# Kernel tuning notes

Hardware: AMD Instinct MI355X
Metric: run time of the kernel (lower is better)

## Reference

```python
import jax, jax.numpy as jnp
import numpy as np

D = 128
N = 768
EPS = 1e-5

def _layernorm(x, w, b):
    m = jnp.mean(x, axis=-1, keepdims=True)
    v = jnp.mean(jnp.square(x - m), axis=-1, keepdims=True)
    return (x - m) * jax.lax.rsqrt(v + EPS) * w + b

def _linear(x, w, b):
    # torch Linear convention: w is [out, in]
    return jnp.einsum('...i,oi->...o', x, w) + b

def setup_inputs() -> dict:
    key = jax.random.key(0)
    ks = jax.random.split(key, 8)
    s = 1.0 / np.sqrt(D)
    d = {
        'pair': jax.random.normal(ks[0], (N, N, D), dtype=jnp.float32),
        'ln_in_w': jnp.ones((D,), jnp.float32), 'ln_in_b': jnp.zeros((D,), jnp.float32),
        'lp_w': jax.random.uniform(ks[1], (D, D), jnp.float32, -s, s), 'lp_b': jnp.zeros((D,), jnp.float32),
        'lg_w': jax.random.uniform(ks[2], (D, D), jnp.float32, -s, s), 'lg_b': jnp.zeros((D,), jnp.float32),
        'rp_w': jax.random.uniform(ks[3], (D, D), jnp.float32, -s, s), 'rp_b': jnp.zeros((D,), jnp.float32),
        'rg_w': jax.random.uniform(ks[4], (D, D), jnp.float32, -s, s), 'rg_b': jnp.zeros((D,), jnp.float32),
        'cn_w': jnp.ones((D,), jnp.float32), 'cn_b': jnp.zeros((D,), jnp.float32),
        'op_w': jax.random.uniform(ks[5], (D, D), jnp.float32, -s, s), 'op_b': jnp.zeros((D,), jnp.float32),
        'og_w': jax.random.uniform(ks[6], (D, D), jnp.float32, -s, s), 'og_b': jnp.zeros((D,), jnp.float32),
        'ln_out_w': jnp.ones((D,), jnp.float32), 'ln_out_b': jnp.zeros((D,), jnp.float32),
    }
    return d

def reference(pair, ln_in_w, ln_in_b, lp_w, lp_b, lg_w, lg_b, rp_w, rp_b, rg_w, rg_b,
              cn_w, cn_b, op_w, op_b, og_w, og_b, ln_out_w, ln_out_b):
    z = _layernorm(pair, ln_in_w, ln_in_b)
    left = jax.nn.sigmoid(_linear(z, lg_w, lg_b)) * _linear(z, lp_w, lp_b)
    right = jax.nn.sigmoid(_linear(z, rg_w, rg_b)) * _linear(z, rp_w, rp_b)
    # outgoing direction: pair(i,j) = sum_k left(i,k,d) * right(j,k,d)
    tri = jnp.einsum('ikd,jkd->ijd', left, right)
    tri = _layernorm(tri, cn_w, cn_b)
    tri = jax.nn.sigmoid(_linear(pair, og_w, og_b)) * _linear(tri, op_w, op_b)
    return _layernorm(pair + tri, ln_out_w, ln_out_b)
```

## Files before the change

kernel.cpp:

```cpp
#include <hip/hip_runtime.h>

#define N 768
#define D 128
#define NSQ (N*N)
#define EPS 1e-5f

typedef __bf16 bf16;
typedef __bf16 bf16x4 __attribute__((ext_vector_type(4)));
typedef __bf16 bf16x8 __attribute__((ext_vector_type(8)));
typedef float f32x4 __attribute__((ext_vector_type(4)));

__device__ __forceinline__ void gld16(const void* g, void* l) {
    __builtin_amdgcn_global_load_lds(
        (const __attribute__((address_space(1))) unsigned int*)g,
        (__attribute__((address_space(3))) unsigned int*)l, 16, 0, 0);
}

__global__ void k_convert_w(const float* __restrict__ lp, const float* __restrict__ lg,
                            const float* __restrict__ rp, const float* __restrict__ rg,
                            const float* __restrict__ op, const float* __restrict__ og,
                            bf16* __restrict__ dst) {
    const float* srcs[6] = {lp, lg, rp, rg, op, og};
    int m = blockIdx.y;
    int i = blockIdx.x * 256 + threadIdx.x;
    dst[m * 16384 + i] = (bf16)srcs[m][i];
}

__global__ __launch_bounds__(512, 2) void k_ln_gate2(
    const float* __restrict__ pair, const float* __restrict__ lnw, const float* __restrict__ lnb,
    const bf16* __restrict__ wbf,
    const float* __restrict__ lp_b, const float* __restrict__ lg_b,
    const float* __restrict__ rp_b, const float* __restrict__ rg_b,
    bf16* __restrict__ left_t, bf16* __restrict__ right_t)
{
    __shared__ bf16 zt[2][64 * 128];

    const int t = threadIdx.x;
    const int lane = t & 63, wid = t >> 6;
    const int side = wid >> 2, dq = wid & 3;
    const int lr = lane & 15, lh = lane >> 4;

    const bf16* wPsrc = wbf + (side ? 2 : 0) * 16384;
    const bf16* wGsrc = wbf + (side ? 3 : 1) * 16384;
    const float* bPp = side ? rp_b : lp_b;
    const float* bGp = side ? rg_b : lg_b;
    bf16* dst = side ? right_t : left_t;

    bf16x8 aP[4][2], aG[4][2];
    #pragma unroll
    for (int kk = 0; kk < 4; ++kk)
        #pragma unroll
        for (int m = 0; m < 2; ++m) {
            int rd = dq * 32 + m * 16 + lr;
            aP[kk][m] = *(const bf16x8*)(wPsrc + rd * 128 + (kk * 4 + lh) * 8);
            aG[kk][m] = *(const bf16x8*)(wGsrc + rd * 128 + (kk * 4 + lh) * 8);
        }
    float bP[2], bG[2];
    #pragma unroll
    for (int m = 0; m < 2; ++m) {
        bP[m] = bPp[dq * 32 + m * 16 + lr];
        bG[m] = bGp[dq * 32 + m * 16 + lr];
    }

    const int r8 = t >> 3, q = t & 7;

    f32x4 lw0 = *(const f32x4*)(lnw + q * 16);
    f32x4 lw1 = *(const f32x4*)(lnw + q * 16 + 4);
    f32x4 lw2 = *(const f32x4*)(lnw + q * 16 + 8);
    f32x4 lw3 = *(const f32x4*)(lnw + q * 16 + 12);
    f32x4 lb0 = *(const f32x4*)(lnb + q * 16);
    f32x4 lb1 = *(const f32x4*)(lnb + q * 16 + 4);
    f32x4 lb2 = *(const f32x4*)(lnb + q * 16 + 8);
    f32x4 lb3 = *(const f32x4*)(lnb + q * 16 + 12);

    const int bid = blockIdx.x, gstride = gridDim.x;

    f32x4 p0, p1, p2, p3;
    {
        const float* prow = pair + (size_t)(bid * 64 + r8) * 128 + q * 16;
        p0 = *(const f32x4*)(prow);
        p1 = *(const f32x4*)(prow + 4);
        p2 = *(const f32x4*)(prow + 8);
        p3 = *(const f32x4*)(prow + 12);
    }

    int buf = 0;
    for (int tile = bid; tile < NSQ / 64; tile += gstride) {
        const int row0 = tile * 64;

        float x[16];
        #pragma unroll
        for (int e = 0; e < 4; ++e) {
            x[e] = p0[e]; x[4 + e] = p1[e]; x[8 + e] = p2[e]; x[12 + e] = p3[e];
        }
        float s1 = 0.f, s2 = 0.f;
        #pragma unroll
        for (int j = 0; j < 16; ++j) { s1 += x[j]; s2 += x[j] * x[j]; }
        s1 += __shfl_xor(s1, 1); s2 += __shfl_xor(s2, 1);
        s1 += __shfl_xor(s1, 2); s2 += __shfl_xor(s2, 2);
        s1 += __shfl_xor(s1, 4); s2 += __shfl_xor(s2, 4);
        float mean = s1 * (1.f / 128.f);
        float rstd = rsqrtf(s2 * (1.f / 128.f) - mean * mean + EPS);

        bf16x8 pk0, pk1;
        #pragma unroll
        for (int e = 0; e < 4; ++e) {
            pk0[e]     = (bf16)((x[e]      - mean) * rstd * lw0[e] + lb0[e]);
            pk0[4 + e] = (bf16)((x[4 + e]  - mean) * rstd * lw1[e] + lb1[e]);
            pk1[e]     = (bf16)((x[8 + e]  - mean) * rstd * lw2[e] + lb2[e]);
            pk1[4 + e] = (bf16)((x[12 + e] - mean) * rstd * lw3[e] + lb3[e]);
        }
        {
            char* zb = (char*)&zt[buf][0];
            *(bf16x8*)(zb + r8 * 256 + ((q * 2)     ^ (r8 & 7)) * 16) = pk0;
            *(bf16x8*)(zb + r8 * 256 + ((q * 2 + 1) ^ (r8 & 7)) * 16) = pk1;
        }
        __syncthreads();

        int nt = tile + gstride;
        if (nt < NSQ / 64) {
            const float* prow = pair + (size_t)(nt * 64 + r8) * 128 + q * 16;
            p0 = *(const f32x4*)(prow);
            p1 = *(const f32x4*)(prow + 4);
            p2 = *(const f32x4*)(prow + 8);
            p3 = *(const f32x4*)(prow + 12);
        }

        f32x4 accP[2][4] = {};
        f32x4 accG[2][4] = {};
        const char* zb = (const char*)&zt[buf][0];
        #pragma unroll
        for (int kk = 0; kk < 4; ++kk) {
            bf16x8 bz[4];
            #pragma unroll
            for (int n = 0; n < 4; ++n) {
                int rz = n * 16 + lr;
                bz[n] = *(const bf16x8*)(zb + rz * 256 + (((kk * 4 + lh)) ^ (rz & 7)) * 16);
            }
            #pragma unroll
            for (int m = 0; m < 2; ++m)
                #pragma unroll
                for (int n = 0; n < 4; ++n) {
                    accP[m][n] = __builtin_amdgcn_mfma_f32_16x16x32_bf16(bz[n], aP[kk][m], accP[m][n], 0, 0, 0);
                    accG[m][n] = __builtin_amdgcn_mfma_f32_16x16x32_bf16(bz[n], aG[kk][m], accG[m][n], 0, 0, 0);
                }
        }

        #pragma unroll
        for (int m = 0; m < 2; ++m) {
            const int d = dq * 32 + m * 16 + lr;
            bf16* drow = dst + (size_t)d * NSQ + row0 + lh * 4;
            #pragma unroll
            for (int n = 0; n < 4; ++n) {
                bf16x4 pk;
                #pragma unroll
                for (int reg = 0; reg < 4; ++reg) {
                    float g = accG[m][n][reg] + bG[m];
                    float p = accP[m][n][reg] + bP[m];
                    pk[reg] = (bf16)(p * (1.f / (1.f + __expf(-g))));
                }
                *(bf16x4*)(drow + n * 16) = pk;
            }
        }
        buf ^= 1;
        __syncthreads();
    }
}

__global__ __launch_bounds__(256, 4) void k_tri(
    const bf16* __restrict__ left_t, const bf16* __restrict__ right_t, bf16* __restrict__ tri_t)
{
    __shared__ bf16 at[2][128 * 32];
    __shared__ bf16 bt[2][128 * 32];
    const int t = threadIdx.x;
    const int b = blockIdx.x;
    const int xcd = b & 7;
    const int s = b >> 3;
    const int d = xcd * 16 + s / 36;
    const int tile = s % 36;
    const int ti = tile / 6, tj = tile % 6;
    const bf16* A = left_t + (size_t)d * NSQ;
    const bf16* B = right_t + (size_t)d * NSQ;
    const int i0 = ti * 128, j0 = tj * 128;

    auto stage = [&](int buf, int kt) {
        int k0 = kt * 32;
        #pragma unroll
        for (int c = 0; c < 2; ++c) {
            int sl = c * 256 + t;
            int r = sl >> 2, cp = sl & 3, cl = cp ^ ((r >> 1) & 3);
            gld16(A + (size_t)(i0 + r) * 768 + k0 + cl * 8, (char*)at[buf] + sl * 16);
            gld16(B + (size_t)(j0 + r) * 768 + k0 + cl * 8, (char*)bt[buf] + sl * 16);
        }
    };

    const int lane = t & 63, wid = t >> 6;
    const int wr = wid >> 1, wc = wid & 1;
    const int lr = lane & 15, lh = lane >> 4;

    f32x4 acc[4][4] = {};

    stage(0, 0);
    for (int kt = 0; kt < 24; ++kt) {
        const int buf = kt & 1;
        asm volatile("s_waitcnt vmcnt(0)" ::: "memory");
        __builtin_amdgcn_s_barrier();

        const bf16* ab = at[buf];
        const bf16* bb = bt[buf];
        bf16x8 af[4], bff[4];
        #pragma unroll
        for (int m = 0; m < 4; ++m) {
            int r = wr * 64 + m * 16 + lr;
            int phys = lh ^ ((r >> 1) & 3);
            af[m] = *(const bf16x8*)((const char*)ab + r * 64 + phys * 16);
        }
        #pragma unroll
        for (int n = 0; n < 4; ++n) {
            int r = wc * 64 + n * 16 + lr;
            int phys = lh ^ ((r >> 1) & 3);
            bff[n] = *(const bf16x8*)((const char*)bb + r * 64 + phys * 16);
        }

        if (kt < 23) stage(buf ^ 1, kt + 1);

        #pragma unroll
        for (int m = 0; m < 4; ++m)
            #pragma unroll
            for (int n = 0; n < 4; ++n)
                acc[m][n] = __builtin_amdgcn_mfma_f32_16x16x32_bf16(bff[n], af[m], acc[m][n], 0, 0, 0);
    }

    bf16* C = tri_t + (size_t)d * NSQ;
    #pragma unroll
    for (int m = 0; m < 4; ++m) {
        const int ri = i0 + wr * 64 + m * 16 + lr;
        bf16* crow = C + (size_t)ri * 768 + j0 + wc * 64 + lh * 4;
        #pragma unroll
        for (int n = 0; n < 4; ++n) {
            bf16x4 pk;
            #pragma unroll
            for (int reg = 0; reg < 4; ++reg)
                pk[reg] = (bf16)acc[m][n][reg];
            *(bf16x4*)(crow + n * 16) = pk;
        }
    }
}

__global__ __launch_bounds__(256, 2) void k_cln(
    const bf16* __restrict__ tri_t, const float* __restrict__ cnw, const float* __restrict__ cnb,
    bf16* __restrict__ tri_ln)
{
    __shared__ bf16 tile[256 * 128];
    __shared__ float mrs[256][2];
    const int t = threadIdx.x;
    const size_t ij = (size_t)blockIdx.x * 256 + t;
    float s1 = 0.f, s2 = 0.f;
    for (int dc = 0; dc < 16; ++dc) {
        bf16x8 pk;
        #pragma unroll
        for (int e = 0; e < 8; ++e) {
            int dd = dc * 8 + e;
            bf16 raw = tri_t[(size_t)dd * NSQ + ij];
            float v = (float)raw;
            s1 += v; s2 += v * v;
            pk[e] = raw;
        }
        *(bf16x8*)((char*)tile + t * 256 + (dc ^ (t & 7)) * 16) = pk;
    }
    float mean = s1 * (1.f / 128.f);
    float rstd = rsqrtf(s2 * (1.f / 128.f) - mean * mean + EPS);
    mrs[t][0] = mean; mrs[t][1] = rstd;
    __syncthreads();
    const size_t ij0 = (size_t)blockIdx.x * 256;
    #pragma unroll
    for (int c = 0; c < 16; ++c) {
        int sl = c * 256 + t;
        int rl = sl >> 4, cp = sl & 15, cl = cp ^ (rl & 7);
        bf16x8 raw = *(const bf16x8*)((const char*)tile + rl * 256 + cp * 16);
        float m = mrs[rl][0], r = mrs[rl][1];
        f32x4 w0 = *(const f32x4*)(cnw + cl * 8);
        f32x4 w1 = *(const f32x4*)(cnw + cl * 8 + 4);
        f32x4 b0 = *(const f32x4*)(cnb + cl * 8);
        f32x4 b1 = *(const f32x4*)(cnb + cl * 8 + 4);
        bf16x8 o;
        #pragma unroll
        for (int e = 0; e < 4; ++e) {
            o[e]     = (bf16)(((float)raw[e]     - m) * r * w0[e] + b0[e]);
            o[4 + e] = (bf16)(((float)raw[4 + e] - m) * r * w1[e] + b1[e]);
        }
        *(bf16x8*)(tri_ln + (ij0 + rl) * 128 + cl * 8) = o;
    }
}

__global__ __launch_bounds__(512, 2) void k_final2(
    const float* __restrict__ pair, const bf16* __restrict__ tri_ln,
    const bf16* __restrict__ wbf,
    const float* __restrict__ op_b, const float* __restrict__ og_b,
    const float* __restrict__ lnow, const float* __restrict__ lnob,
    float* __restrict__ out)
{
    __shared__ bf16 zt[64 * 128];
    __shared__ bf16 tt[2][64 * 128];
    __shared__ bf16 ub[64 * 136];

    const int t = threadIdx.x;
    const int lane = t & 63, wid = t >> 6;
    const int dq = wid & 3, wh = wid >> 2;
    const int lr = lane & 15, lh = lane >> 4;

    const bf16* opsrc = wbf + 4 * 16384;
    const bf16* ogsrc = wbf + 5 * 16384;

    bf16x8 aOG[4][2], aOP[4][2];
    #pragma unroll
    for (int kk = 0; kk < 4; ++kk)
        #pragma unroll
        for (int m = 0; m < 2; ++m) {
            int rd = dq * 32 + m * 16 + lr;
            aOG[kk][m] = *(const bf16x8*)(ogsrc + rd * 128 + (kk * 4 + lh) * 8);
            aOP[kk][m] = *(const bf16x8*)(opsrc + rd * 128 + (kk * 4 + lh) * 8);
        }
    f32x4 vbOG[2], vbOP[2];
    #pragma unroll
    for (int m = 0; m < 2; ++m) {
        vbOG[m] = *(const f32x4*)(og_b + dq * 32 + m * 16 + lh * 4);
        vbOP[m] = *(const f32x4*)(op_b + dq * 32 + m * 16 + lh * 4);
    }

    const int r8 = t >> 3, q = t & 7;
    f32x4 lw0 = *(const f32x4*)(lnow + q * 16);
    f32x4 lw1 = *(const f32x4*)(lnow + q * 16 + 4);
    f32x4 lw2 = *(const f32x4*)(lnow + q * 16 + 8);
    f32x4 lw3 = *(const f32x4*)(lnow + q * 16 + 12);
    f32x4 lb0 = *(const f32x4*)(lnob + q * 16);
    f32x4 lb1 = *(const f32x4*)(lnob + q * 16 + 4);
    f32x4 lb2 = *(const f32x4*)(lnob + q * 16 + 8);
    f32x4 lb3 = *(const f32x4*)(lnob + q * 16 + 12);

    const int bid = blockIdx.x, gstride = gridDim.x;

    auto stage_tt = [&](int buf, int tile) {
        const int row0 = tile * 64;
        #pragma unroll
        for (int c = 0; c < 2; ++c) {
            int s = c * 512 + t;
            int r = s >> 4, cp = s & 15, cl = cp ^ (r & 7);
            gld16(tri_ln + (size_t)(row0 + r) * 128 + cl * 8, (char*)tt[buf] + s * 16);
        }
    };

    f32x4 pA0, pA1, pA2, pA3;
    {
        const float* prow = pair + (size_t)(bid * 64 + r8) * 128 + q * 16;
        pA0 = *(const f32x4*)(prow);
        pA1 = *(const f32x4*)(prow + 4);
        pA2 = *(const f32x4*)(prow + 8);
        pA3 = *(const f32x4*)(prow + 12);
    }
    stage_tt(0, bid);

    int buf = 0;
    for (int tile = bid; tile < NSQ / 64; tile += gstride) {
        const int row0 = tile * 64;

        {
            bf16x8 pk0, pk1;
            #pragma unroll
            for (int e = 0; e < 4; ++e) {
                pk0[e]     = (bf16)pA0[e];
                pk0[4 + e] = (bf16)pA1[e];
                pk1[e]     = (bf16)pA2[e];
                pk1[4 + e] = (bf16)pA3[e];
            }
            char* zb = (char*)zt;
            *(bf16x8*)(zb + r8 * 256 + ((q * 2)     ^ (r8 & 7)) * 16) = pk0;
            *(bf16x8*)(zb + r8 * 256 + ((q * 2 + 1) ^ (r8 & 7)) * 16) = pk1;
        }
        __syncthreads();

        const int nt = tile + gstride;
        if (nt < NSQ / 64) stage_tt(buf ^ 1, nt);

        f32x4 pB0 = pA0, pB1 = pA1, pB2 = pA2, pB3 = pA3;
        if (nt < NSQ / 64) {
            const float* prow = pair + (size_t)(nt * 64 + r8) * 128 + q * 16;
            pB0 = *(const f32x4*)(prow);
            pB1 = *(const f32x4*)(prow + 4);
            pB2 = *(const f32x4*)(prow + 8);
            pB3 = *(const f32x4*)(prow + 12);
        }

        f32x4 accOG[2][2] = {};
        f32x4 accOP[2][2] = {};
        const char* zb = (const char*)zt;
        const char* tb = (const char*)tt[buf];
        #pragma unroll
        for (int kk = 0; kk < 4; ++kk) {
            bf16x8 bzp[2], bzt[2];
            #pragma unroll
            for (int n = 0; n < 2; ++n) {
                int rz = wh * 32 + n * 16 + lr;
                int phys = (kk * 4 + lh) ^ (rz & 7);
                bzp[n] = *(const bf16x8*)(zb + rz * 256 + phys * 16);
                bzt[n] = *(const bf16x8*)(tb + rz * 256 + phys * 16);
            }
            #pragma unroll
            for (int m = 0; m < 2; ++m)
                #pragma unroll
                for (int n = 0; n < 2; ++n) {
                    accOG[m][n] = __builtin_amdgcn_mfma_f32_16x16x32_bf16(aOG[kk][m], bzp[n], accOG[m][n], 0, 0, 0);
                    accOP[m][n] = __builtin_amdgcn_mfma_f32_16x16x32_bf16(aOP[kk][m], bzt[n], accOP[m][n], 0, 0, 0);
                }
        }

        #pragma unroll
        for (int m = 0; m < 2; ++m)
            #pragma unroll
            for (int n = 0; n < 2; ++n) {
                int rr = wh * 32 + n * 16 + lr;
                bf16x4 v;
                #pragma unroll
                for (int reg = 0; reg < 4; ++reg) {
                    float g = accOG[m][n][reg] + vbOG[m][reg];
                    float p = accOP[m][n][reg] + vbOP[m][reg];
                    v[reg] = (bf16)(p * (1.f / (1.f + __expf(-g))));
                }
                *(bf16x4*)(ub + rr * 136 + dq * 32 + m * 16 + lh * 4) = v;
            }
        __syncthreads();

        {
            float x[16];
            const bf16* ur = ub + r8 * 136 + q * 16;
            bf16x8 u0 = *(const bf16x8*)(ur);
            bf16x8 u1 = *(const bf16x8*)(ur + 8);
            #pragma unroll
            for (int e = 0; e < 4; ++e) {
                x[e]      = pA0[e] + (float)u0[e];
                x[4 + e]  = pA1[e] + (float)u0[4 + e];
                x[8 + e]  = pA2[e] + (float)u1[e];
                x[12 + e] = pA3[e] + (float)u1[4 + e];
            }
            float s1 = 0.f, s2 = 0.f;
            #pragma unroll
            for (int j = 0; j < 16; ++j) { s1 += x[j]; s2 += x[j] * x[j]; }
            s1 += __shfl_xor(s1, 1); s2 += __shfl_xor(s2, 1);
            s1 += __shfl_xor(s1, 2); s2 += __shfl_xor(s2, 2);
            s1 += __shfl_xor(s1, 4); s2 += __shfl_xor(s2, 4);
            float mean = s1 * (1.f / 128.f);
            float rstd = rsqrtf(s2 * (1.f / 128.f) - mean * mean + EPS);
            float* orow = out + (size_t)(row0 + r8) * 128 + q * 16;
            f32x4 o0, o1, o2, o3;
            #pragma unroll
            for (int e = 0; e < 4; ++e) {
                o0[e] = (x[e]      - mean) * rstd * lw0[e] + lb0[e];
                o1[e] = (x[4 + e]  - mean) * rstd * lw1[e] + lb1[e];
                o2[e] = (x[8 + e]  - mean) * rstd * lw2[e] + lb2[e];
                o3[e] = (x[12 + e] - mean) * rstd * lw3[e] + lb3[e];
            }
            *(f32x4*)(orow)      = o0;
            *(f32x4*)(orow + 4)  = o1;
            *(f32x4*)(orow + 8)  = o2;
            *(f32x4*)(orow + 12) = o3;
        }

        pA0 = pB0; pA1 = pB1; pA2 = pB2; pA3 = pB3;
        buf ^= 1;
    }
}

extern "C" void kernel_launch(void* const* d_in, const int* in_sizes, int n_in,
                              void* d_out, int out_size, void* d_ws, size_t ws_size,
                              hipStream_t stream) {
    const float* pair    = (const float*)d_in[0];
    const float* ln_in_w = (const float*)d_in[1];
    const float* ln_in_b = (const float*)d_in[2];
    const float* lp_w    = (const float*)d_in[3];
    const float* lp_b    = (const float*)d_in[4];
    const float* lg_w    = (const float*)d_in[5];
    const float* lg_b    = (const float*)d_in[6];
    const float* rp_w    = (const float*)d_in[7];
    const float* rp_b    = (const float*)d_in[8];
    const float* rg_w    = (const float*)d_in[9];
    const float* rg_b    = (const float*)d_in[10];
    const float* cn_w    = (const float*)d_in[11];
    const float* cn_b    = (const float*)d_in[12];
    const float* op_w    = (const float*)d_in[13];
    const float* op_b    = (const float*)d_in[14];
    const float* og_w    = (const float*)d_in[15];
    const float* og_b    = (const float*)d_in[16];
    const float* ln_out_w = (const float*)d_in[17];
    const float* ln_out_b = (const float*)d_in[18];

    const size_t HALF = (size_t)128 * NSQ * 2;
    char* ws = (char*)d_ws;
    bf16* wbf     = (bf16*)ws;
    bf16* right_t = (bf16*)(ws + 196608);
    bf16* tri_ln  = right_t;
    bf16* left_t  = (bf16*)d_out;
    bf16* tri_t   = (bf16*)((char*)d_out + HALF);

    k_convert_w<<<dim3(64, 6), 256, 0, stream>>>(lp_w, lg_w, rp_w, rg_w, op_w, og_w, wbf);
    k_ln_gate2<<<dim3(512), 512, 0, stream>>>(pair, ln_in_w, ln_in_b, wbf,
                                              lp_b, lg_b, rp_b, rg_b, left_t, right_t);
    k_tri<<<dim3(4608), 256, 0, stream>>>(left_t, right_t, tri_t);
    k_cln<<<dim3(NSQ / 256), 256, 0, stream>>>(tri_t, cn_w, cn_b, tri_ln);
    k_final2<<<dim3(512), 512, 0, stream>>>(pair, tri_ln, wbf, op_b, og_b,
                                            ln_out_w, ln_out_b, (float*)d_out);
}
```

Baseline: 586.6 us.

## Fuse center layernorm into final kernel and replace syncthreads with LDS barriers

Removes the separate k_cln kernel. The final kernel now gathers the d-major tri_t tile itself, transposes it through LDS, applies the center layernorm in place, and prefetches the next tile into registers while the MFMAs run. This saves a full write and read of the normalized tri tensor in HBM and one kernel launch. It also drops a trailing __syncthreads in k_ln_gate2 and uses lgkmcnt-only barriers. That risks LDS hazards, and the strided 2-byte gathers from tri_t may coalesce poorly. Buffer locations in the workspace and output are also reassigned.

Measured after the change: 587.2 us. About the same (+0.1%).

```diff
diff --git a/kernel.cpp b/kernel.cpp
--- a/kernel.cpp
+++ b/kernel.cpp
@@ -14,6 +14,12 @@
     __builtin_amdgcn_global_load_lds(
         (const __attribute__((address_space(1))) unsigned int*)g,
         (__attribute__((address_space(3))) unsigned int*)l, 16, 0, 0);
+}
+
+__device__ __forceinline__ void barrier_lds() {
+    asm volatile("s_waitcnt lgkmcnt(0)" ::: "memory");
+    __builtin_amdgcn_s_barrier();
+    __builtin_amdgcn_sched_barrier(0);
 }
 
 __global__ void k_convert_w(const float* __restrict__ lp, const float* __restrict__ lg,
@@ -115,7 +121,7 @@
             *(bf16x8*)(zb + r8 * 256 + ((q * 2)     ^ (r8 & 7)) * 16) = pk0;
             *(bf16x8*)(zb + r8 * 256 + ((q * 2 + 1) ^ (r8 & 7)) * 16) = pk1;
         }
-        __syncthreads();
+        barrier_lds();
 
         int nt = tile + gstride;
         if (nt < NSQ / 64) {
@@ -163,7 +169,6 @@
             }
         }
         buf ^= 1;
-        __syncthreads();
     }
 }
 
@@ -247,55 +252,10 @@
     }
 }
 
-__global__ __launch_bounds__(256, 2) void k_cln(
-    const bf16* __restrict__ tri_t, const float* __restrict__ cnw, const float* __restrict__ cnb,
-    bf16* __restrict__ tri_ln)
-{
-    __shared__ bf16 tile[256 * 128];
-    __shared__ float mrs[256][2];
-    const int t = threadIdx.x;
-    const size_t ij = (size_t)blockIdx.x * 256 + t;
-    float s1 = 0.f, s2 = 0.f;
-    for (int dc = 0; dc < 16; ++dc) {
-        bf16x8 pk;
-        #pragma unroll
-        for (int e = 0; e < 8; ++e) {
-            int dd = dc * 8 + e;
-            bf16 raw = tri_t[(size_t)dd * NSQ + ij];
-            float v = (float)raw;
-            s1 += v; s2 += v * v;
-            pk[e] = raw;
-        }
-        *(bf16x8*)((char*)tile + t * 256 + (dc ^ (t & 7)) * 16) = pk;
-    }
-    float mean = s1 * (1.f / 128.f);
-    float rstd = rsqrtf(s2 * (1.f / 128.f) - mean * mean + EPS);
-    mrs[t][0] = mean; mrs[t][1] = rstd;
-    __syncthreads();
-    const size_t ij0 = (size_t)blockIdx.x * 256;
-    #pragma unroll
-    for (int c = 0; c < 16; ++c) {
-        int sl = c * 256 + t;
-        int rl = sl >> 4, cp = sl & 15, cl = cp ^ (rl & 7);
-        bf16x8 raw = *(const bf16x8*)((const char*)tile + rl * 256 + cp * 16);
-        float m = mrs[rl][0], r = mrs[rl][1];
-        f32x4 w0 = *(const f32x4*)(cnw + cl * 8);
-        f32x4 w1 = *(const f32x4*)(cnw + cl * 8 + 4);
-        f32x4 b0 = *(const f32x4*)(cnb + cl * 8);
-        f32x4 b1 = *(const f32x4*)(cnb + cl * 8 + 4);
-        bf16x8 o;
-        #pragma unroll
-        for (int e = 0; e < 4; ++e) {
-            o[e]     = (bf16)(((float)raw[e]     - m) * r * w0[e] + b0[e]);
-            o[4 + e] = (bf16)(((float)raw[4 + e] - m) * r * w1[e] + b1[e]);
-        }
-        *(bf16x8*)(tri_ln + (ij0 + rl) * 128 + cl * 8) = o;
-    }
-}
-
-__global__ __launch_bounds__(512, 2) void k_final2(
-    const float* __restrict__ pair, const bf16* __restrict__ tri_ln,
+__global__ __launch_bounds__(512, 2) void k_final3(
+    const float* __restrict__ pair, const bf16* __restrict__ tri_t,
     const bf16* __restrict__ wbf,
+    const float* __restrict__ cn_w, const float* __restrict__ cn_b,
     const float* __restrict__ op_b, const float* __restrict__ og_b,
     const float* __restrict__ lnow, const float* __restrict__ lnob,
     float* __restrict__ out)
@@ -338,18 +298,21 @@
     f32x4 lb2 = *(const f32x4*)(lnob + q * 16 + 8);
     f32x4 lb3 = *(const f32x4*)(lnob + q * 16 + 12);
 
+    const int ijl = t & 63, g = t >> 6;
     const int bid = blockIdx.x, gstride = gridDim.x;
 
-    auto stage_tt = [&](int buf, int tile) {
-        const int row0 = tile * 64;
-        #pragma unroll
-        for (int c = 0; c < 2; ++c) {
-            int s = c * 512 + t;
-            int r = s >> 4, cp = s & 15, cl = cp ^ (r & 7);
-            gld16(tri_ln + (size_t)(row0 + r) * 128 + cl * 8, (char*)tt[buf] + s * 16);
-        }
-    };
-
+    {
+        const int r0 = bid * 64;
+        #pragma unroll
+        for (int h = 0; h < 2; ++h) {
+            const int do8 = g + 8 * h;
+            bf16x8 v;
+            #pragma unroll
+            for (int e = 0; e < 8; ++e)
+                v[e] = tri_t[(size_t)(do8 * 8 + e) * NSQ + r0 + ijl];
+            *(bf16x8*)((char*)tt[0] + ijl * 256 + ((do8 ^ (ijl & 7)) * 16)) = v;
+        }
+    }
     f32x4 pA0, pA1, pA2, pA3;
     {
         const float* prow = pair + (size_t)(bid * 64 + r8) * 128 + q * 16;
@@ -358,7 +321,6 @@
         pA2 = *(const f32x4*)(prow + 8);
         pA3 = *(const f32x4*)(prow + 12);
     }
-    stage_tt(0, bid);
 
     int buf = 0;
     for (int tile = bid; tile < NSQ / 64; tile += gstride) {
@@ -377,11 +339,9 @@
             *(bf16x8*)(zb + r8 * 256 + ((q * 2)     ^ (r8 & 7)) * 16) = pk0;
             *(bf16x8*)(zb + r8 * 256 + ((q * 2 + 1) ^ (r8 & 7)) * 16) = pk1;
         }
-        __syncthreads();
+        barrier_lds();
 
         const int nt = tile + gstride;
-        if (nt < NSQ / 64) stage_tt(buf ^ 1, nt);
-
         f32x4 pB0 = pA0, pB1 = pA1, pB2 = pA2, pB3 = pA3;
         if (nt < NSQ / 64) {
             const float* prow = pair + (size_t)(nt * 64 + r8) * 128 + q * 16;
@@ -391,6 +351,55 @@
             pB3 = *(const f32x4*)(prow + 12);
         }
 
+        {
+            char* tb = (char*)tt[buf];
+            const int c0 = (2 * q) ^ (r8 & 7), c1 = (2 * q + 1) ^ (r8 & 7);
+            bf16x8 x0 = *(const bf16x8*)(tb + r8 * 256 + c0 * 16);
+            bf16x8 x1 = *(const bf16x8*)(tb + r8 * 256 + c1 * 16);
+            float f[16];
+            float s1 = 0.f, s2 = 0.f;
+            #pragma unroll
+            for (int e = 0; e < 8; ++e) {
+                f[e] = (float)x0[e]; f[8 + e] = (float)x1[e];
+            }
+            #pragma unroll
+            for (int j = 0; j < 16; ++j) { s1 += f[j]; s2 += f[j] * f[j]; }
+            s1 += __shfl_xor(s1, 1); s2 += __shfl_xor(s2, 1);
+            s1 += __shfl_xor(s1, 2); s2 += __shfl_xor(s2, 2);
+            s1 += __shfl_xor(s1, 4); s2 += __shfl_xor(s2, 4);
+            float mean = s1 * (1.f / 128.f);
+            float rstd = rsqrtf(s2 * (1.f / 128.f) - mean * mean + EPS);
+            f32x4 w00 = *(const f32x4*)(cn_w + q * 16);
+            f32x4 w01 = *(const f32x4*)(cn_w + q * 16 + 4);
+            f32x4 w10 = *(const f32x4*)(cn_w + q * 16 + 8);
+            f32x4 w11 = *(const f32x4*)(cn_w + q * 16 + 12);
+            f32x4 b00 = *(const f32x4*)(cn_b + q * 16);
+            f32x4 b01 = *(const f32x4*)(cn_b + q * 16 + 4);
+            f32x4 b10 = *(const f32x4*)(cn_b + q * 16 + 8);
+            f32x4 b11 = *(const f32x4*)(cn_b + q * 16 + 12);
+            bf16x8 o0, o1;
+            #pragma unroll
+            for (int e = 0; e < 4; ++e) {
+                o0[e]     = (bf16)((f[e]      - mean) * rstd * w00[e] + b00[e]);
+                o0[4 + e] = (bf16)((f[4 + e]  - mean) * rstd * w01[e] + b01[e]);
+                o1[e]     = (bf16)((f[8 + e]  - mean) * rstd * w10[e] + b10[e]);
+                o1[4 + e] = (bf16)((f[12 + e] - mean) * rstd * w11[e] + b11[e]);
+            }
+            *(bf16x8*)(tb + r8 * 256 + c0 * 16) = o0;
+            *(bf16x8*)(tb + r8 * 256 + c1 * 16) = o1;
+        }
+        barrier_lds();
+
+        bf16x8 nv0, nv1;
+        if (nt < NSQ / 64) {
+            const int r0 = nt * 64;
+            #pragma unroll
+            for (int e = 0; e < 8; ++e) {
+                nv0[e] = tri_t[(size_t)(g * 8 + e) * NSQ + r0 + ijl];
+                nv1[e] = tri_t[(size_t)((g + 8) * 8 + e) * NSQ + r0 + ijl];
+            }
+        }
+
         f32x4 accOG[2][2] = {};
         f32x4 accOP[2][2] = {};
         const char* zb = (const char*)zt;
@@ -414,6 +423,11 @@
                 }
         }
 
+        if (nt < NSQ / 64) {
+            *(bf16x8*)((char*)tt[buf ^ 1] + ijl * 256 + ((g       ^ (ijl & 7)) * 16)) = nv0;
+            *(bf16x8*)((char*)tt[buf ^ 1] + ijl * 256 + (((g + 8) ^ (ijl & 7)) * 16)) = nv1;
+        }
+
         #pragma unroll
         for (int m = 0; m < 2; ++m)
             #pragma unroll
@@ -422,13 +436,13 @@
                 bf16x4 v;
                 #pragma unroll
                 for (int reg = 0; reg < 4; ++reg) {
-                    float g = accOG[m][n][reg] + vbOG[m][reg];
-                    float p = accOP[m][n][reg] + vbOP[m][reg];
-                    v[reg] = (bf16)(p * (1.f / (1.f + __expf(-g))));
+                    float gg = accOG[m][n][reg] + vbOG[m][reg];
+                    float p  = accOP[m][n][reg] + vbOP[m][reg];
+                    v[reg] = (bf16)(p * (1.f / (1.f + __expf(-gg))));
                 }
                 *(bf16x4*)(ub + rr * 136 + dq * 32 + m * 16 + lh * 4) = v;
             }
-        __syncthreads();
+        barrier_lds();
 
         {
             float x[16];
@@ -496,16 +510,14 @@
     const size_t HALF = (size_t)128 * NSQ * 2;
     char* ws = (char*)d_ws;
     bf16* wbf     = (bf16*)ws;
-    bf16* right_t = (bf16*)(ws + 196608);
-    bf16* tri_ln  = right_t;
+    bf16* tri_t   = (bf16*)(ws + 196608);
     bf16* left_t  = (bf16*)d_out;
-    bf16* tri_t   = (bf16*)((char*)d_out + HALF);
+    bf16* right_t = (bf16*)((char*)d_out + HALF);
 
     k_convert_w<<<dim3(64, 6), 256, 0, stream>>>(lp_w, lg_w, rp_w, rg_w, op_w, og_w, wbf);
     k_ln_gate2<<<dim3(512), 512, 0, stream>>>(pair, ln_in_w, ln_in_b, wbf,
                                               lp_b, lg_b, rp_b, rg_b, left_t, right_t);
     k_tri<<<dim3(4608), 256, 0, stream>>>(left_t, right_t, tri_t);
-    k_cln<<<dim3(NSQ / 256), 256, 0, stream>>>(tri_t, cn_w, cn_b, tri_ln);
-    k_final2<<<dim3(512), 512, 0, stream>>>(pair, tri_ln, wbf, op_b, og_b,
-                                            ln_out_w, ln_out_b, (float*)d_out);
-}
+    k_final3<<<dim3(512), 512, 0, stream>>>(pair, tri_t, wbf, cn_w, cn_b,
+                                            op_b, og_b, ln_out_w, ln_out_b, (float*)d_out);
+}
```
